# Kernel optimization log

Hardware: AMD Instinct MI355X
Metric: run time of the kernel (lower is better)

## Reference

```python
import jax, jax.numpy as jnp
import numpy as np

B, T, IN_DIM, H, C = 2048, 512, 28, 64, 10


def setup_inputs() -> dict:
    key = jax.random.key(0)
    ks = jax.random.split(key, 7)
    s = 1.0 / np.sqrt(H)  # PyTorch RNN init scale
    u = lambda k, shape: jax.random.uniform(k, shape, jnp.float32, -s, s)
    return {
        "x": jax.random.normal(ks[0], (B, 1, T, IN_DIM), jnp.float32),
        "W_ih": u(ks[1], (3 * H, IN_DIM)),  # gates ordered (r, z, n)
        "W_hh": u(ks[2], (3 * H, H)),
        "b_ih": u(ks[3], (3 * H,)),
        "b_hh": u(ks[4], (3 * H,)),
        "W_out": u(ks[5], (C, H)),
        "b_out": u(ks[6], (C,)),
    }


def reference(x, W_ih, W_hh, b_ih, b_hh, W_out, b_out):
    x = x[:, 0]  # squeeze(1) -> [B, T, IN]
    # Precompute all input-to-gate projections once: [B, T, 3H]
    xg = jnp.einsum("bti,gi->btg", x, W_ih) + b_ih

    def step(h, xg_t):
        gh = h @ W_hh.T + b_hh                      # [B, 3H]
        xr, xz, xn = jnp.split(xg_t, 3, axis=-1)
        hr, hz, hn = jnp.split(gh, 3, axis=-1)
        r = jax.nn.sigmoid(xr + hr)
        z = jax.nn.sigmoid(xz + hz)
        n = jnp.tanh(xn + r * hn)
        h_new = (1.0 - z) * n + z * h
        return h_new, None

    h0 = jnp.zeros((x.shape[0], H), x.dtype)
    hT, _ = jax.lax.scan(step, h0, jnp.swapaxes(xg, 0, 1))  # scan over time
    logits = hT @ W_out.T + b_out                            # [B, C]
    return jax.nn.softmax(logits, axis=-1)
```

## Files before the change

kernel.cpp:

```cpp
#include <hip/hip_runtime.h>

#define BB     2048
#define TT     512
#define INDIM  28
#define HH     64
#define NC     10
#define ROWS   16
#define NTHREADS 256
#define LDA    104

typedef __attribute__((ext_vector_type(8))) _Float16 f16x8;
typedef __attribute__((ext_vector_type(4))) float     f32x4;

__device__ __forceinline__ float frcp(float v)  { return __builtin_amdgcn_rcpf(v); }
__device__ __forceinline__ float fsig(float v)  { return frcp(1.f + __expf(-v)); }
__device__ __forceinline__ float ftanh_(float v){ return fmaf(-2.f, frcp(1.f + __expf(2.f*v)), 1.f); }

#define MFMA(A_, B_, C_) __builtin_amdgcn_mfma_f32_16x16x32_f16((A_), (B_), (C_), 0, 0, 0)

__device__ __forceinline__ void lds_barrier() {
    asm volatile("s_waitcnt lgkmcnt(0)" ::: "memory");
    __builtin_amdgcn_s_barrier();
}

extern "C" __global__ __launch_bounds__(NTHREADS, 1)
void gru_mfma(const float* __restrict__ x,
              const float* __restrict__ W_ih,
              const float* __restrict__ W_hh,
              const float* __restrict__ b_ih,
              const float* __restrict__ b_hh,
              const float* __restrict__ W_out,
              const float* __restrict__ b_out,
              float* __restrict__ out)
{
    __shared__ __align__(16) _Float16 A_[2][16][LDA];
    __shared__ float hs_f[ROWS][HH];
    __shared__ float lg[ROWS][NC];

    const int tid = threadIdx.x;
    const int w   = tid >> 6;
    const int l   = tid & 63;
    const int c   = l & 15;
    const int hi  = l >> 4;
    const int hi8 = hi * 8;
    const int u   = w * 16 + c;
    const int r0  = blockIdx.x * ROWS;

    f16x8 Bh[9];
    {
        const int GS[9][2] = {{0,0},{0,1},{0,2},{1,0},{1,1},{1,2},{2,0},{2,1},{3,2}};
        #pragma unroll
        for (int f = 0; f < 9; ++f) {
            const int g = GS[f][0], s = GS[f][1];
            #pragma unroll
            for (int j = 0; j < 8; ++j) {
                const int k = s * 32 + hi8 + j;
                float v = 0.f;
                if (g == 2)      { if (k < 64) v = W_hh[(size_t)(u + 128) * HH + k]; }
                else if (g == 3) { if (k >= 64 && k < 64 + INDIM) v = W_ih[(size_t)(u + 128) * INDIM + (k - 64)]; }
                else {
                    const int ru = u + 64 * g;
                    if (k < 64)              v = W_hh[(size_t)ru * HH + k];
                    else if (k < 64 + INDIM) v = W_ih[(size_t)ru * INDIM + (k - 64)];
                }
                Bh[f][j] = (_Float16)v;
            }
        }
    }
    const float bs0  = b_ih[u]       + b_hh[u];
    const float bs1  = b_ih[u + 64]  + b_hh[u + 64];
    const float bihn = b_ih[u + 128];
    const float bhhn = b_hh[u + 128];

    for (int i = tid; i < 2 * 16 * LDA; i += NTHREADS) ((_Float16*)A_)[i] = (_Float16)0.f;

    const int  row0 = tid / INDIM,          col0 = tid % INDIM;
    const bool a1   = tid < (ROWS * INDIM - NTHREADS);
    const int  e1   = tid + NTHREADS;
    const int  row1 = a1 ? (e1 / INDIM) : 0, col1 = a1 ? (e1 % INDIM) : 0;
    const float* xb0 = x + (size_t)(r0 + row0) * TT * INDIM + col0;
    const float* xb1 = x + (size_t)(r0 + row1) * TT * INDIM + col1;

    A_[0][row0][64 + col0] = (_Float16)xb0[0];
    if (a1) A_[0][row1][64 + col1] = (_Float16)xb1[0];
    float xg0[8], xg1[8];
    #pragma unroll
    for (int k = 0; k < 8; ++k) {
        xg0[k] = xb0[(size_t)(1 + k) * INDIM];
        xg1[k] = a1 ? xb1[(size_t)(1 + k) * INDIM] : 0.f;
    }
    __syncthreads();

    float h[4] = {0.f, 0.f, 0.f, 0.f};
    const f32x4 z4 = {0.f, 0.f, 0.f, 0.f};
    int p = 0;

    for (int g = 0; g < TT / 8; ++g) {
        float xn0[8], xn1[8];
        #pragma unroll
        for (int k = 0; k < 8; ++k) {
            const int st = 8 * (g + 1) + 1 + k;
            const bool ok = st < TT;
            xn0[k] = ok ? xb0[(size_t)st * INDIM] : 0.f;
            xn1[k] = (ok && a1) ? xb1[(size_t)st * INDIM] : 0.f;
        }

        #pragma unroll
        for (int k = 0; k < 8; ++k) {
            const int t = 8 * g + k;

            const f16x8 af0 = *(const f16x8*)&A_[p][c][hi8];
            const f16x8 af1 = *(const f16x8*)&A_[p][c][32 + hi8];
            const f16x8 af2 = *(const f16x8*)&A_[p][c][64 + hi8];

            f32x4 a0 = MFMA(af0, Bh[0], z4);
            f32x4 a1v = MFMA(af0, Bh[3], z4);
            f32x4 a2 = MFMA(af0, Bh[6], z4);
            a0  = MFMA(af1, Bh[1], a0);
            a1v = MFMA(af1, Bh[4], a1v);
            a2  = MFMA(af1, Bh[7], a2);
            a0  = MFMA(af2, Bh[2], a0);
            a1v = MFMA(af2, Bh[5], a1v);
            f32x4 a3 = MFMA(af2, Bh[8], z4);

            #pragma unroll
            for (int i = 0; i < 4; ++i) {
                const float rg = fsig(a0[i] + bs0);
                const float zg = fsig(a1v[i] + bs1);
                const float ng = ftanh_(a3[i] + bihn + rg * (a2[i] + bhhn));
                h[i] = fmaf(zg, h[i] - ng, ng);
            }
            #pragma unroll
            for (int i = 0; i < 4; ++i)
                A_[p ^ 1][4 * hi + i][u] = (_Float16)h[i];
            if (t + 1 < TT) {
                A_[p ^ 1][row0][64 + col0] = (_Float16)xg0[k];
                if (a1) A_[p ^ 1][row1][64 + col1] = (_Float16)xg1[k];
            }
            lds_barrier();
            p ^= 1;
        }
        #pragma unroll
        for (int k = 0; k < 8; ++k) { xg0[k] = xn0[k]; xg1[k] = xn1[k]; }
    }

    #pragma unroll
    for (int i = 0; i < 4; ++i) hs_f[4 * hi + i][u] = h[i];
    __syncthreads();
    if (tid < ROWS * NC) {
        const int rr = tid / NC, cc = tid % NC;
        float s = b_out[cc];
        const float* wo = W_out + (size_t)cc * HH;
        #pragma unroll
        for (int j = 0; j < HH; ++j) s = fmaf(wo[j], hs_f[rr][j], s);
        lg[rr][cc] = s;
    }
    __syncthreads();
    if (tid < ROWS) {
        float mx = -1e30f;
        #pragma unroll
        for (int cc = 0; cc < NC; ++cc) mx = fmaxf(mx, lg[tid][cc]);
        float e[NC]; float ssum = 0.f;
        #pragma unroll
        for (int cc = 0; cc < NC; ++cc) { e[cc] = __expf(lg[tid][cc] - mx); ssum += e[cc]; }
        const float inv = 1.f / ssum;
        float* op = out + (size_t)(r0 + tid) * NC;
        #pragma unroll
        for (int cc = 0; cc < NC; ++cc) op[cc] = e[cc] * inv;
    }
}

extern "C" void kernel_launch(void* const* d_in, const int* in_sizes, int n_in,
                              void* d_out, int out_size, void* d_ws, size_t ws_size,
                              hipStream_t stream) {
    const float* x     = (const float*)d_in[0];
    const float* W_ih  = (const float*)d_in[1];
    const float* W_hh  = (const float*)d_in[2];
    const float* b_ih  = (const float*)d_in[3];
    const float* b_hh  = (const float*)d_in[4];
    const float* W_out = (const float*)d_in[5];
    const float* b_out = (const float*)d_in[6];
    (void)in_sizes; (void)n_in; (void)d_ws; (void)ws_size; (void)out_size;

    gru_mfma<<<BB / ROWS, NTHREADS, 0, stream>>>(x, W_ih, W_hh, b_ih, b_hh,
                                                 W_out, b_out, (float*)d_out);
}
```

Before: 223.6 us.

## Transpose GRU MFMA operands, feed x from registers, fold biases into accumulators

The MFMA operands are swapped so the weights are the A operand and the hidden state is B. Each lane now owns four consecutive hidden units of one batch row, which lets the new h be written to LDS as a single packed f16x4 store. The x inputs are loaded straight from global memory into registers as float4 and converted to the f16 fragment in place, so x is no longer staged through LDS. Biases are used as the initial MFMA accumulators, which removes the per-step bias adds. In exchange the prefetch buffer grows to 16 float4 registers per lane, and the x loads are now issued right before the per-step barrier.

```diff
diff --git a/kernel.cpp b/kernel.cpp
--- a/kernel.cpp
+++ b/kernel.cpp
@@ -7,9 +7,10 @@
 #define NC     10
 #define ROWS   16
 #define NTHREADS 256
-#define LDA    104
+#define LDH    104
 
 typedef __attribute__((ext_vector_type(8))) _Float16 f16x8;
+typedef __attribute__((ext_vector_type(4))) _Float16 f16x4;
 typedef __attribute__((ext_vector_type(4))) float     f32x4;
 
 __device__ __forceinline__ float frcp(float v)  { return __builtin_amdgcn_rcpf(v); }
@@ -33,7 +34,7 @@
               const float* __restrict__ b_out,
               float* __restrict__ out)
 {
-    __shared__ __align__(16) _Float16 A_[2][16][LDA];
+    __shared__ __align__(16) _Float16 H_[2][16][LDH];
     __shared__ float hs_f[ROWS][HH];
     __shared__ float lg[ROWS][NC];
 
@@ -44,6 +45,7 @@
     const int hi  = l >> 4;
     const int hi8 = hi * 8;
     const int u   = w * 16 + c;
+    const int u0  = w * 16 + 4 * hi;
     const int r0  = blockIdx.x * ROWS;
 
     f16x8 Bh[9];
@@ -67,85 +69,77 @@
             }
         }
     }
-    const float bs0  = b_ih[u]       + b_hh[u];
-    const float bs1  = b_ih[u + 64]  + b_hh[u + 64];
-    const float bihn = b_ih[u + 128];
-    const float bhhn = b_hh[u + 128];
+    f32x4 bv_r, bv_z, bv_nh, bv_nx;
+    #pragma unroll
+    for (int i = 0; i < 4; ++i) {
+        bv_r[i]  = b_ih[u0 + i]       + b_hh[u0 + i];
+        bv_z[i]  = b_ih[u0 + i + 64]  + b_hh[u0 + i + 64];
+        bv_nh[i] = b_hh[u0 + i + 128];
+        bv_nx[i] = b_ih[u0 + i + 128];
+    }
 
-    for (int i = tid; i < 2 * 16 * LDA; i += NTHREADS) ((_Float16*)A_)[i] = (_Float16)0.f;
+    for (int i = tid; i < 2 * 16 * LDH; i += NTHREADS) ((_Float16*)H_)[i] = (_Float16)0.f;
 
-    const int  row0 = tid / INDIM,          col0 = tid % INDIM;
-    const bool a1   = tid < (ROWS * INDIM - NTHREADS);
-    const int  e1   = tid + NTHREADS;
-    const int  row1 = a1 ? (e1 / INDIM) : 0, col1 = a1 ? (e1 % INDIM) : 0;
-    const float* xb0 = x + (size_t)(r0 + row0) * TT * INDIM + col0;
-    const float* xb1 = x + (size_t)(r0 + row1) * TT * INDIM + col1;
-
-    A_[0][row0][64 + col0] = (_Float16)xb0[0];
-    if (a1) A_[0][row1][64 + col1] = (_Float16)xb1[0];
-    float xg0[8], xg1[8];
+    const float* xlane = x + (size_t)(r0 + c) * (size_t)TT * INDIM + hi8;
+    const float4 zf4 = {0.f, 0.f, 0.f, 0.f};
+    float4 xa[8], xb[8];
     #pragma unroll
     for (int k = 0; k < 8; ++k) {
-        xg0[k] = xb0[(size_t)(1 + k) * INDIM];
-        xg1[k] = a1 ? xb1[(size_t)(1 + k) * INDIM] : 0.f;
+        xa[k] = *(const float4*)(xlane + (size_t)k * INDIM);
+        xb[k] = (hi < 3) ? *(const float4*)(xlane + (size_t)k * INDIM + 4) : zf4;
     }
     __syncthreads();
 
     float h[4] = {0.f, 0.f, 0.f, 0.f};
-    const f32x4 z4 = {0.f, 0.f, 0.f, 0.f};
     int p = 0;
 
     for (int g = 0; g < TT / 8; ++g) {
-        float xn0[8], xn1[8];
-        #pragma unroll
-        for (int k = 0; k < 8; ++k) {
-            const int st = 8 * (g + 1) + 1 + k;
-            const bool ok = st < TT;
-            xn0[k] = ok ? xb0[(size_t)st * INDIM] : 0.f;
-            xn1[k] = (ok && a1) ? xb1[(size_t)st * INDIM] : 0.f;
-        }
-
         #pragma unroll
         for (int k = 0; k < 8; ++k) {
             const int t = 8 * g + k;
 
-            const f16x8 af0 = *(const f16x8*)&A_[p][c][hi8];
-            const f16x8 af1 = *(const f16x8*)&A_[p][c][32 + hi8];
-            const f16x8 af2 = *(const f16x8*)&A_[p][c][64 + hi8];
+            f16x8 xf;
+            {
+                const float v[8] = {xa[k].x, xa[k].y, xa[k].z, xa[k].w,
+                                    xb[k].x, xb[k].y, xb[k].z, xb[k].w};
+                #pragma unroll
+                for (int j = 0; j < 8; ++j) xf[j] = (_Float16)v[j];
+            }
+            const f16x8 bf0 = *(const f16x8*)&H_[p][c][hi8];
+            const f16x8 bf1 = *(const f16x8*)&H_[p][c][32 + hi8];
 
-            f32x4 a0 = MFMA(af0, Bh[0], z4);
-            f32x4 a1v = MFMA(af0, Bh[3], z4);
-            f32x4 a2 = MFMA(af0, Bh[6], z4);
-            a0  = MFMA(af1, Bh[1], a0);
-            a1v = MFMA(af1, Bh[4], a1v);
-            a2  = MFMA(af1, Bh[7], a2);
-            a0  = MFMA(af2, Bh[2], a0);
-            a1v = MFMA(af2, Bh[5], a1v);
-            f32x4 a3 = MFMA(af2, Bh[8], z4);
+            f32x4 a0 = MFMA(Bh[0], bf0, bv_r);
+            f32x4 a1 = MFMA(Bh[3], bf0, bv_z);
+            f32x4 a2 = MFMA(Bh[6], bf0, bv_nh);
+            a0 = MFMA(Bh[1], bf1, a0);
+            a1 = MFMA(Bh[4], bf1, a1);
+            a2 = MFMA(Bh[7], bf1, a2);
+            a0 = MFMA(Bh[2], xf, a0);
+            a1 = MFMA(Bh[5], xf, a1);
+            f32x4 a3 = MFMA(Bh[8], xf, bv_nx);
 
+            f16x4 hv;
             #pragma unroll
             for (int i = 0; i < 4; ++i) {
-                const float rg = fsig(a0[i] + bs0);
-                const float zg = fsig(a1v[i] + bs1);
-                const float ng = ftanh_(a3[i] + bihn + rg * (a2[i] + bhhn));
+                const float rg = fsig(a0[i]);
+                const float zg = fsig(a1[i]);
+                const float ng = ftanh_(fmaf(rg, a2[i], a3[i]));
                 h[i] = fmaf(zg, h[i] - ng, ng);
+                hv[i] = (_Float16)h[i];
             }
-            #pragma unroll
-            for (int i = 0; i < 4; ++i)
-                A_[p ^ 1][4 * hi + i][u] = (_Float16)h[i];
-            if (t + 1 < TT) {
-                A_[p ^ 1][row0][64 + col0] = (_Float16)xg0[k];
-                if (a1) A_[p ^ 1][row1][64 + col1] = (_Float16)xg1[k];
+            *(f16x4*)&H_[p ^ 1][c][u0] = hv;
+
+            if (t + 8 < TT) {
+                xa[k] = *(const float4*)(xlane + (size_t)(t + 8) * INDIM);
+                if (hi < 3) xb[k] = *(const float4*)(xlane + (size_t)(t + 8) * INDIM + 4);
             }
             lds_barrier();
             p ^= 1;
         }
-        #pragma unroll
-        for (int k = 0; k < 8; ++k) { xg0[k] = xn0[k]; xg1[k] = xn1[k]; }
     }
 
     #pragma unroll
-    for (int i = 0; i < 4; ++i) hs_f[4 * hi + i][u] = h[i];
+    for (int i = 0; i < 4; ++i) hs_f[c][u0 + i] = h[i];
     __syncthreads();
     if (tid < ROWS * NC) {
         const int rr = tid / NC, cc = tid % NC;
```

Measured after the change: 199.3 us. -10.9%, faster.
